# Optimization experiments

Hardware: AMD Instinct MI355X
Metric: run time of the kernel (lower is better)

## Reference

```python
import jax, jax.numpy as jnp
import numpy as np

N_FEAT = 64      # number of continuous features
N_BINS = 255     # bin edges per feature (EBM default) -> 256 score slots incl. OOV
N_PAIRS = 32     # interaction terms
BATCH = 262144


def _bin_indices(edges, x):
    """TF Discretization (searchsorted right) + IntegerLookup(vocab=range(B), OOV->0).
    edges: [N, B] sorted per row; x: [batch, N] -> int32 [batch, N] in [0, B]."""
    idx = jax.vmap(lambda e, col: jnp.searchsorted(e, col, side='right'),
                   in_axes=(0, 1), out_axes=1)(edges, x)  # [batch, N], values 0..B
    B = edges.shape[1]
    # IntegerLookup: value v in {0..B-1} -> v+1 ; value B (not in vocab) -> OOV index 0
    return jnp.where(idx < B, idx + 1, 0)


def setup_inputs() -> dict:
    key = jax.random.key(0)
    ks = jax.random.split(key, 6)
    x = jax.random.normal(ks[0], (BATCH, N_FEAT), dtype=jnp.float32)
    edges = jnp.sort(jax.random.normal(ks[1], (N_FEAT, N_BINS), dtype=jnp.float32), axis=1)
    pair_edges = jnp.sort(jax.random.normal(ks[2], (N_FEAT, N_BINS), dtype=jnp.float32), axis=1)
    w = jax.random.normal(ks[3], (N_FEAT, N_BINS + 1), dtype=jnp.float32) * 0.1
    tables = jax.random.normal(ks[4], (N_PAIRS, N_BINS + 1, N_BINS + 1), dtype=jnp.float32) * 0.1
    pairs = jax.random.randint(ks[5], (N_PAIRS, 2), 0, N_FEAT, dtype=jnp.int32)
    bias = jnp.zeros((1,), dtype=jnp.float32)
    return {"x": x, "edges": edges, "w": w, "pair_edges": pair_edges,
            "pairs": pairs, "tables": tables, "bias": bias}


def reference(x, edges, w, pair_edges, pairs, tables, bias):
    # --- per-feature main effects: one_hot(idx) @ Dense(1) == gather w[f, idx] ---
    idx = _bin_indices(edges, x)                                  # [batch, N]
    feat = w[jnp.arange(N_FEAT)[None, :], idx]                    # [batch, N]
    # --- pairwise interactions: gather_nd on [L, R] lookup tables ---
    pidx = _bin_indices(pair_edges, x)                            # [batch, N]
    li = pidx[:, pairs[:, 0]]                                     # [batch, P]
    ri = pidx[:, pairs[:, 1]]                                     # [batch, P]
    inter = tables[jnp.arange(N_PAIRS)[None, :], li, ri]          # [batch, P]
    # --- BiasLayer: reduce_sum(concat, axis=1) + bias, then sigmoid ---
    logits = jnp.sum(feat, axis=1) + jnp.sum(inter, axis=1) + bias[0]
    return jax.nn.sigmoid(logits)                                  # [batch]
```

## Files before the change

### kernel.cpp

```cpp
#include <hip/hip_runtime.h>
#include <hip/hip_fp16.h>

#define NBINS 255
#define NPAIRS 32
#define BIGF 3.0e38f


__global__ void ebm_prep(const float* __restrict__ edges,
                         const float* __restrict__ pair_edges,
                         const float* __restrict__ w,
                         float* __restrict__ ws) {
    int tid = blockIdx.x * blockDim.x + threadIdx.x;
    int f = tid >> 8, j = tid & 255;
    float* E  = ws;
    float* PE = ws + 16384;
    float* ME = ws + 32768;
    float* MP = ws + 36864;
    float* CU = ws + 40960;
    float* CP = ws + 41984;
    __half* W = (__half*)(ws + 43008);
    E[tid]  = (j < NBINS) ? edges[f * NBINS + j]      : BIGF;
    PE[tid] = (j < NBINS) ? pair_edges[f * NBINS + j] : BIGF;
    int src = (j < 255) ? j + 1 : 0;
    W[tid]  = __float2half(w[f * 256 + src]);
    if (j < 64) {
        int idx = 4 * j + 3;
        ME[f * 64 + j] = (idx < NBINS) ? edges[f * NBINS + idx]      : BIGF;
        MP[f * 64 + j] = (idx < NBINS) ? pair_edges[f * NBINS + idx] : BIGF;
    }
    if (j < 16) {
        CU[f * 16 + j] = (j < 15) ? edges[f * NBINS + 16 * j + 15]      : BIGF;
        CP[f * 16 + j] = (j < 15) ? pair_edges[f * NBINS + 16 * j + 15] : BIGF;
    }
}

__global__ void ebm_prep_tables(const float* __restrict__ tables,
                                unsigned short* __restrict__ o) {
    int i = blockIdx.x * blockDim.x + threadIdx.x;
    int b = i & 255, a = (i >> 8) & 255, p = i >> 16;
    int ra = (a < 255) ? a + 1 : 0;
    int rb = (b < 255) ? b + 1 : 0;
    o[i] = __half_as_ushort(__float2half(tables[(p << 16) + (ra << 8) + rb]));
}

__device__ __forceinline__ unsigned pick16(const unsigned* pw, int s) {
    unsigned v01 = (s & 1) ? pw[1]  : pw[0];
    unsigned v23 = (s & 1) ? pw[3]  : pw[2];
    unsigned v45 = (s & 1) ? pw[5]  : pw[4];
    unsigned v67 = (s & 1) ? pw[7]  : pw[6];
    unsigned v89 = (s & 1) ? pw[9]  : pw[8];
    unsigned vab = (s & 1) ? pw[11] : pw[10];
    unsigned vcd = (s & 1) ? pw[13] : pw[12];
    unsigned vef = (s & 1) ? pw[15] : pw[14];
    unsigned w0 = (s & 2) ? v23 : v01;
    unsigned w1 = (s & 2) ? v67 : v45;
    unsigned w2 = (s & 2) ? vab : v89;
    unsigned w3 = (s & 2) ? vef : vcd;
    unsigned u0 = (s & 4) ? w1 : w0;
    unsigned u1 = (s & 4) ? w3 : w2;
    return (s & 8) ? u1 : u0;
}

__global__ __launch_bounds__(1024) void ebm_main(
    const float* __restrict__ x,
    const int*   __restrict__ pairs,
    const float* __restrict__ tables_f32,
    const float* __restrict__ bias,
    const float* __restrict__ ws,
    const __half* __restrict__ T16,
    int useT16,
    float*       __restrict__ out) {

    __shared__ float  sE[16384];
    __shared__ float  sPE[16384];
    __shared__ float4 sME[1024];
    __shared__ float4 sMP[1024];

    int tid = threadIdx.x;
    {
        const float4* w4 = (const float4*)ws;
        float4* dE = (float4*)sE;
        float4* dP = (float4*)sPE;
        for (int i = tid; i < 4096; i += 1024) {
            dE[i] = w4[i];
            dP[i] = w4[4096 + i];
        }
        if (tid < 1024) {
            sME[tid] = w4[8192 + tid];
            sMP[tid] = w4[9216 + tid];
        }
    }
    const float*  CU = ws + 40960;
    const float*  CP = ws + 41984;
    const __half* Wg = (const __half*)(ws + 43008);
    float bias0 = bias[0];

    __syncthreads();

    int row = blockIdx.x * 1024 + tid;
    const float4* x4 = (const float4*)x + row * 16;
    const float4* sE4 = (const float4*)sE;
    const float4* sP4 = (const float4*)sPE;

    float acc = 0.f;
    unsigned pw[16];

    float4 xg = x4[0];
#pragma unroll
    for (int g = 0; g < 16; ++g) {
        float4 xnext = xg;
        if (g < 15) xnext = x4[g + 1];
        float xf[4] = {xg.x, xg.y, xg.z, xg.w};

        int t[4];
#pragma unroll
        for (int j = 0; j < 4; ++j) {
            const float* cu = CU + (4 * g + j) * 16;
            int tt = 0;
#pragma unroll
            for (int k = 0; k < 15; ++k) tt += (xf[j] >= cu[k]);
            t[j] = tt;
        }
        int t2[4];
#pragma unroll
        for (int j = 0; j < 4; ++j) {
            const float* cp = CP + (4 * g + j) * 16;
            int tt = 0;
#pragma unroll
            for (int k = 0; k < 15; ++k) tt += (xf[j] >= cp[k]);
            t2[j] = tt;
        }
        float4 mu[4], mp[4];
#pragma unroll
        for (int j = 0; j < 4; ++j) mu[j] = sME[(4 * g + j) * 16 + t[j]];
#pragma unroll
        for (int j = 0; j < 4; ++j) mp[j] = sMP[(4 * g + j) * 16 + t2[j]];
        int lo[4], lo2[4];
        float4 fu[4], fp[4];
#pragma unroll
        for (int j = 0; j < 4; ++j) {
            int m = (xf[j] >= mu[j].x) + (xf[j] >= mu[j].y) + (xf[j] >= mu[j].z);
            lo[j] = 4 * t[j] + m;
            fu[j] = sE4[(4 * g + j) * 64 + lo[j]];
        }
#pragma unroll
        for (int j = 0; j < 4; ++j) {
            int m = (xf[j] >= mp[j].x) + (xf[j] >= mp[j].y) + (xf[j] >= mp[j].z);
            lo2[j] = 4 * t2[j] + m;
            fp[j] = sP4[(4 * g + j) * 64 + lo2[j]];
        }
#pragma unroll
        for (int j = 0; j < 4; ++j) {
            int c = 4 * lo[j] + (xf[j] >= fu[j].x) + (xf[j] >= fu[j].y) +
                    (xf[j] >= fu[j].z) + (xf[j] >= fu[j].w);
            acc += __half2float(Wg[(4 * g + j) * 256 + c]);
        }
        unsigned pword = 0;
#pragma unroll
        for (int j = 0; j < 4; ++j) {
            int c2 = 4 * lo2[j] + (xf[j] >= fp[j].x) + (xf[j] >= fp[j].y) +
                     (xf[j] >= fp[j].z) + (xf[j] >= fp[j].w);
            pword |= (unsigned)c2 << (8 * j);
        }
        pw[g] = pword;
        xg = xnext;
    }

    if (useT16) {
#pragma unroll
        for (int p = 0; p < NPAIRS; ++p) {
            int a = pairs[2 * p], b = pairs[2 * p + 1];
            unsigned wa = pick16(pw, a >> 2);
            unsigned wb = pick16(pw, b >> 2);
            int li = (wa >> ((a & 3) * 8)) & 255;
            int ri = (wb >> ((b & 3) * 8)) & 255;
            acc += __half2float(T16[(p << 16) + (li << 8) + ri]);
        }
    } else {
#pragma unroll
        for (int p = 0; p < NPAIRS; ++p) {
            int a = pairs[2 * p], b = pairs[2 * p + 1];
            unsigned wa = pick16(pw, a >> 2);
            unsigned wb = pick16(pw, b >> 2);
            int li = (wa >> ((a & 3) * 8)) & 255;
            int ri = (wb >> ((b & 3) * 8)) & 255;
            int lb = (li < 255) ? li + 1 : 0;
            int rb = (ri < 255) ? ri + 1 : 0;
            acc += tables_f32[(p << 16) + (lb << 8) + rb];
        }
    }

    out[row] = 1.0f / (1.0f + __expf(-(acc + bias0)));
}

extern "C" void kernel_launch(void* const* d_in, const int* in_sizes, int n_in,
                              void* d_out, int out_size, void* d_ws, size_t ws_size,
                              hipStream_t stream) {
    const float* x          = (const float*)d_in[0];
    const float* edges      = (const float*)d_in[1];
    const float* w          = (const float*)d_in[2];
    const float* pair_edges = (const float*)d_in[3];
    const int*   pairs      = (const int*)d_in[4];
    const float* tables     = (const float*)d_in[5];
    const float* bias       = (const float*)d_in[6];
    float* out = (float*)d_out;
    float* ws  = (float*)d_ws;

    int useT16 = (ws_size >= (size_t)4399104) ? 1 : 0;
    __half* T16 = (__half*)((char*)d_ws + 204800);

    ebm_prep<<<64, 256, 0, stream>>>(edges, pair_edges, w, ws);
    if (useT16) {
        ebm_prep_tables<<<2048, 1024, 0, stream>>>(tables, (unsigned short*)T16);
    }
    ebm_main<<<256, 1024, 0, stream>>>(x, pairs, tables, bias, ws, T16, useT16, out);
}
```

Measured before the change: 193.7 us.

## Split EBM into per-feature-quarter binning kernel and separate pair-lookup kernel

Replaces the single 1024-thread kernel with two stages. The first stage splits the 64 features into quarters across blocks, so each block stages less shared memory and more blocks can be resident. It also skips pair-edge binning for features that no pair uses, and writes partial sums and packed bin indices to workspace. The second stage reads these back, unpacks the bytes through shared memory and does the table gathers, at the cost of extra global traffic and an extra launch, and it runs only when the workspace is large enough.

```diff
diff --git a/kernel.cpp b/kernel.cpp
--- a/kernel.cpp
+++ b/kernel.cpp
@@ -43,6 +43,152 @@
     o[i] = __half_as_ushort(__float2half(tables[(p << 16) + (ra << 8) + rb]));
 }
 
+__global__ __launch_bounds__(512, 8) void ebm_bins(
+    const float* __restrict__ x,
+    const int*   __restrict__ pairs,
+    float* ws) {
+
+    __shared__ float  sE[4096];
+    __shared__ float  sPE[4096];
+    __shared__ float4 sME[256];
+    __shared__ float4 sMP[256];
+
+    int tid = threadIdx.x;
+    int q  = blockIdx.x & 3;
+    int row = (blockIdx.x >> 2) * 512 + tid;
+    int f0 = q * 16;
+
+    const float4* w4 = (const float4*)ws;
+    {
+        float4* dE = (float4*)sE;
+        float4* dP = (float4*)sPE;
+        dE[tid]       = w4[f0 * 64 + tid];
+        dE[tid + 512] = w4[f0 * 64 + tid + 512];
+        dP[tid]       = w4[4096 + f0 * 64 + tid];
+        dP[tid + 512] = w4[4096 + f0 * 64 + tid + 512];
+        if (tid < 256) {
+            sME[tid] = w4[8192 + f0 * 16 + tid];
+            sMP[tid] = w4[9216 + f0 * 16 + tid];
+        }
+    }
+
+    unsigned long long mask = 0;
+#pragma unroll 1
+    for (int k = 0; k < 2 * NPAIRS; ++k) mask |= 1ull << pairs[k];
+
+    __syncthreads();
+
+    const float*  CU = ws + 40960;
+    const float*  CP = ws + 41984;
+    const __half* Wg = (const __half*)(ws + 43008);
+    const float4* sE4 = (const float4*)sE;
+    const float4* sP4 = (const float4*)sPE;
+    const float4* x4 = (const float4*)x + (size_t)row * 16;
+
+    float acc = 0.f;
+    unsigned pwq[4];
+
+#pragma unroll
+    for (int g = 0; g < 4; ++g) {
+        float4 xg = x4[q * 4 + g];
+        float xf[4] = {xg.x, xg.y, xg.z, xg.w};
+
+        int t[4];
+#pragma unroll
+        for (int j = 0; j < 4; ++j) {
+            const float* cu = CU + (f0 + 4 * g + j) * 16;
+            int tt = 0;
+#pragma unroll
+            for (int k = 0; k < 15; ++k) tt += (xf[j] >= cu[k]);
+            t[j] = tt;
+        }
+        float4 mu[4];
+#pragma unroll
+        for (int j = 0; j < 4; ++j) mu[j] = sME[(4 * g + j) * 16 + t[j]];
+        int lo[4];
+        float4 fu[4];
+#pragma unroll
+        for (int j = 0; j < 4; ++j) {
+            int m = (xf[j] >= mu[j].x) + (xf[j] >= mu[j].y) + (xf[j] >= mu[j].z);
+            lo[j] = 4 * t[j] + m;
+            fu[j] = sE4[(4 * g + j) * 64 + lo[j]];
+        }
+#pragma unroll
+        for (int j = 0; j < 4; ++j) {
+            int c = 4 * lo[j] + (xf[j] >= fu[j].x) + (xf[j] >= fu[j].y) +
+                    (xf[j] >= fu[j].z) + (xf[j] >= fu[j].w);
+            acc += __half2float(Wg[(f0 + 4 * g + j) * 256 + c]);
+        }
+
+        unsigned pword = 0;
+#pragma unroll
+        for (int j = 0; j < 4; ++j) {
+            int f = f0 + 4 * g + j;
+            if ((mask >> f) & 1) {
+                const float* cp = CP + f * 16;
+                int tt = 0;
+#pragma unroll
+                for (int k = 0; k < 15; ++k) tt += (xf[j] >= cp[k]);
+                float4 mp = sMP[(4 * g + j) * 16 + tt];
+                int m = (xf[j] >= mp.x) + (xf[j] >= mp.y) + (xf[j] >= mp.z);
+                int l2 = 4 * tt + m;
+                float4 fp = sP4[(4 * g + j) * 64 + l2];
+                int c2 = 4 * l2 + (xf[j] >= fp.x) + (xf[j] >= fp.y) +
+                         (xf[j] >= fp.z) + (xf[j] >= fp.w);
+                pword |= (unsigned)c2 << (8 * j);
+            }
+        }
+        pwq[g] = pword;
+    }
+
+    float* P = ws + 51200;
+    P[q * 262144 + row] = acc;
+    unsigned* PW = (unsigned*)(ws + 1099776);
+#pragma unroll
+    for (int g = 0; g < 4; ++g) PW[(q * 4 + g) * 262144 + row] = pwq[g];
+}
+
+__global__ __launch_bounds__(256, 8) void ebm_pairs(
+    const int*   __restrict__ pairs,
+    const float* __restrict__ tables_f32,
+    const float* __restrict__ bias,
+    const float* __restrict__ ws,
+    const __half* __restrict__ T16,
+    int useT16,
+    float* __restrict__ out) {
+
+    __shared__ unsigned char sB[256 * 68];
+    int tid = threadIdx.x;
+    int row = blockIdx.x * 256 + tid;
+
+    const float* P = ws + 51200;
+    float acc = bias[0] + P[row] + P[262144 + row] + P[524288 + row] + P[786432 + row];
+
+    const unsigned* PW = (const unsigned*)(ws + 1099776);
+    unsigned* myw = (unsigned*)(sB + tid * 68);
+#pragma unroll
+    for (int k = 0; k < 16; ++k) myw[k] = PW[k * 262144 + row];
+
+    const unsigned char* me = sB + tid * 68;
+    if (useT16) {
+#pragma unroll
+        for (int p = 0; p < NPAIRS; ++p) {
+            int a = pairs[2 * p], b = pairs[2 * p + 1];
+            int li = me[a], ri = me[b];
+            acc += __half2float(T16[(p << 16) + (li << 8) + ri]);
+        }
+    } else {
+#pragma unroll
+        for (int p = 0; p < NPAIRS; ++p) {
+            int a = pairs[2 * p], b = pairs[2 * p + 1];
+            int li = me[a], ri = me[b];
+            int lb = (li < 255) ? li + 1 : 0, rb = (ri < 255) ? ri + 1 : 0;
+            acc += tables_f32[(p << 16) + (lb << 8) + rb];
+        }
+    }
+    out[row] = 1.0f / (1.0f + __expf(-acc));
+}
+
 __device__ __forceinline__ unsigned pick16(const unsigned* pw, int s) {
     unsigned v01 = (s & 1) ? pw[1]  : pw[0];
     unsigned v23 = (s & 1) ? pw[3]  : pw[2];
@@ -61,7 +207,7 @@
     return (s & 8) ? u1 : u0;
 }
 
-__global__ __launch_bounds__(1024) void ebm_main(
+__global__ __launch_bounds__(1024) void ebm_mono(
     const float* __restrict__ x,
     const int*   __restrict__ pairs,
     const float* __restrict__ tables_f32,
@@ -98,7 +244,7 @@
     __syncthreads();
 
     int row = blockIdx.x * 1024 + tid;
-    const float4* x4 = (const float4*)x + row * 16;
+    const float4* x4 = (const float4*)x + (size_t)row * 16;
     const float4* sE4 = (const float4*)sE;
     const float4* sP4 = (const float4*)sPE;
 
@@ -111,7 +257,6 @@
         float4 xnext = xg;
         if (g < 15) xnext = x4[g + 1];
         float xf[4] = {xg.x, xg.y, xg.z, xg.w};
-
         int t[4];
 #pragma unroll
         for (int j = 0; j < 4; ++j) {
@@ -189,7 +334,6 @@
             acc += tables_f32[(p << 16) + (lb << 8) + rb];
         }
     }
-
     out[row] = 1.0f / (1.0f + __expf(-(acc + bias0)));
 }
 
@@ -206,12 +350,22 @@
     float* out = (float*)d_out;
     float* ws  = (float*)d_ws;
 
-    int useT16 = (ws_size >= (size_t)4399104) ? 1 : 0;
-    __half* T16 = (__half*)((char*)d_ws + 204800);
-
     ebm_prep<<<64, 256, 0, stream>>>(edges, pair_edges, w, ws);
-    if (useT16) {
-        ebm_prep_tables<<<2048, 1024, 0, stream>>>(tables, (unsigned short*)T16);
-    }
-    ebm_main<<<256, 1024, 0, stream>>>(x, pairs, tables, bias, ws, T16, useT16, out);
-}
+
+    if (ws_size >= (size_t)21176320) {
+        int useT16 = (ws_size >= (size_t)25370624) ? 1 : 0;
+        __half* T16 = (__half*)((char*)d_ws + 21176320);
+        if (useT16) {
+            ebm_prep_tables<<<2048, 1024, 0, stream>>>(tables, (unsigned short*)T16);
+        }
+        ebm_bins<<<2048, 512, 0, stream>>>(x, pairs, ws);
+        ebm_pairs<<<1024, 256, 0, stream>>>(pairs, tables, bias, ws, T16, useT16, out);
+    } else {
+        int useT16 = (ws_size >= (size_t)4399104) ? 1 : 0;
+        __half* T16 = (__half*)((char*)d_ws + 204800);
+        if (useT16) {
+            ebm_prep_tables<<<2048, 1024, 0, stream>>>(tables, (unsigned short*)T16);
+        }
+        ebm_mono<<<256, 1024, 0, stream>>>(x, pairs, tables, bias, ws, T16, useT16, out);
+    }
+}
```

Result: slower. 209.0 us (+7.9%).
